# Optimization experiments

Measured on AMD Instinct MI355X. Metric: run time of the kernel, lower is better.

Reference implementation:

```python
import jax, jax.numpy as jnp
import numpy as np


def _to_complex(e):
    # e: [..., L, 2] (real, imag) -> complex64 [..., L]
    return e[..., 0] + 1j * e[..., 1]


def _idct_last(x, expk):
    # IDCT (DCT-III-like, no normalization, full weight on x_0) along last axis:
    #   y_u = sum_{k=0}^{N-1} x_k cos(pi*k*(2u+1)/(2N))
    # Makhoul FFT algorithm: t = N*ifft(x * exp(i*pi*k/(2N)));
    #   y_{2n} = Re t_n, y_{2n+1} = Re t_{N-1-n}
    N = x.shape[-1]
    t = jnp.fft.ifft(x * expk, axis=-1) * N
    re = jnp.real(t).astype(x.dtype)
    y = jnp.zeros_like(x)
    y = y.at[..., 0::2].set(re[..., : (N + 1) // 2])
    y = y.at[..., 1::2].set(re[..., ::-1][..., : N // 2])
    return y


def _idxst_last(x, expk):
    # IDXST along last axis: y_u = sum_{k=0}^{N-1} x_k sin(pi*k*(2u+1)/(2N))
    # Identity: sin(pi*k*(2u+1)/(2N)) = (-1)^u cos(pi*(N-k)*(2u+1)/(2N))
    # => y = (-1)^u * idct(x') with x'_0 = 0, x'_j = x_{N-j}
    N = x.shape[-1]
    xp = jnp.concatenate([jnp.zeros_like(x[..., :1]), x[..., :0:-1]], axis=-1)
    sign = jnp.where(jnp.arange(N) % 2 == 0, 1.0, -1.0).astype(x.dtype)
    return _idct_last(xp, expk) * sign


def setup_inputs() -> dict:
    key = jax.random.key(0)
    M, N = 4096, 4096
    x = jax.random.normal(key, (M, N), dtype=jnp.float32)
    kM = np.arange(M)
    kN = np.arange(N)
    expkM = np.stack([np.cos(np.pi * kM / (2 * M)), np.sin(np.pi * kM / (2 * M))], axis=-1).astype(np.float32)
    expkN = np.stack([np.cos(np.pi * kN / (2 * N)), np.sin(np.pi * kN / (2 * N))], axis=-1).astype(np.float32)
    return {"x": x, "expkM": jnp.asarray(expkM), "expkN": jnp.asarray(expkN)}


def reference(x, expkM, expkN):
    # 2D separable transform: IDXST along dim 0 (M), IDCT along dim 1 (N)
    eM = _to_complex(expkM)
    eN = _to_complex(expkN)
    y = _idxst_last(x.T, eM).T  # idxst over rows (size M)
    y = _idct_last(y, eN)       # idct over cols (size N)
    return y
```

## Files before the change

kernel.cpp:

```cpp
#include <hip/hip_runtime.h>
#include <hip/hip_bf16.h>

typedef __bf16 bf16x8 __attribute__((ext_vector_type(8)));
typedef float  f32x4  __attribute__((ext_vector_type(4)));

__device__ __forceinline__ unsigned short f2bf(float f) {
    union { float f; unsigned int u; } v; v.f = f;
    unsigned int r = v.u + 0x7FFFu + ((v.u >> 16) & 1u);
    return (unsigned short)(r >> 16);
}

__device__ __forceinline__ void async16(const unsigned short* g, unsigned short* l) {
    __builtin_amdgcn_global_load_lds(
        (const __attribute__((address_space(1))) unsigned int*)g,
        (__attribute__((address_space(3))) unsigned int*)l,
        16, 0, 0);
}

__global__ __launch_bounds__(256) void transpose_perm(
    const float* __restrict__ X, unsigned short* __restrict__ Xt, int Mr, int Nc)
{
    __shared__ float tile[64][65];
    const int bx = blockIdx.x * 64;
    const int by = blockIdx.y * 64;
    const int tid = threadIdx.x;
    const int halfM = Mr >> 1;

    const int c4 = (tid & 15) * 4;
    const int r  = tid >> 4;
#pragma unroll
    for (int p = 0; p < 4; ++p) {
        const float4 v = *reinterpret_cast<const float4*>(
            &X[(size_t)(by + r + 16 * p) * Nc + bx + c4]);
        tile[r + 16 * p][c4 + 0] = v.x;
        tile[r + 16 * p][c4 + 1] = v.y;
        tile[r + 16 * p][c4 + 2] = v.z;
        tile[r + 16 * p][c4 + 3] = v.w;
    }
    __syncthreads();

    const int q  = tid & 7;
    const int h  = (tid >> 3) & 1;
    const int n0 = tid >> 4;
#pragma unroll
    for (int p = 0; p < 4; ++p) {
        const int n = n0 + 16 * p;
        ushort4 o;
        o.x = f2bf(tile[8 * q + 0 + h][n]);
        o.y = f2bf(tile[8 * q + 2 + h][n]);
        o.z = f2bf(tile[8 * q + 4 + h][n]);
        o.w = f2bf(tile[8 * q + 6 + h][n]);
        *reinterpret_cast<ushort4*>(
            Xt + (size_t)(bx + n) * Mr + h * halfM + (by >> 1) + 4 * q) = o;
    }
}

__global__ __launch_bounds__(256) void gen_w(
    unsigned short* __restrict__ out, int doSin)
{
    const int flat = (int)(((size_t)blockIdx.x * 256 + threadIdx.x) * 4);
    const int r  = flat >> 12;
    const int c0 = flat & 4095;
    const unsigned int step = 2u * (unsigned int)r + 1u;
    const float scale = 3.14159265358979323846f / 8192.0f;
    unsigned short o[4];
#pragma unroll
    for (int j = 0; j < 4; ++j) {
        const int c = c0 + j;
        const unsigned int kk = (c < 2048) ? (unsigned int)(2 * c)
                                           : (unsigned int)(2 * (c - 2048) + 1);
        unsigned int p = (kk * step) & 16383u;
        float ang = (float)p * scale;
        float v = doSin ? __sinf(ang) : __cosf(ang);
        o[j] = f2bf(v);
    }
    uint2 pack;
    pack.x = (unsigned int)o[0] | ((unsigned int)o[1] << 16);
    pack.y = (unsigned int)o[2] | ((unsigned int)o[3] << 16);
    *reinterpret_cast<uint2*>(out + flat) = pack;
}

#define BARRIER __builtin_amdgcn_s_barrier()
#define LGKM0 asm volatile("s_waitcnt lgkmcnt(0)" ::: "memory")
#define VM6 asm volatile("s_waitcnt vmcnt(6)" ::: "memory")
#define VM0 asm volatile("s_waitcnt vmcnt(0)" ::: "memory")
#define PRIO1 __builtin_amdgcn_s_setprio(1)
#define PRIO0 __builtin_amdgcn_s_setprio(0)

#define STAGE_ALL(LB, KC) do { \
    _Pragma("unroll") for (int U = 0; U < BMU; ++U) \
        async16(pA + (size_t)U * 64 * 4096 + (KC), &lds[(LB) + U * 4096 + ldst]); \
    _Pragma("unroll") for (int U = 0; U < BNU; ++U) \
        async16(pB + (size_t)U * 64 * 4096 + (KC), &lds[(LB) + (BMU + U) * 4096 + ldst]); } while (0)

#define LD_ALL(LB) do { \
    _Pragma("unroll") for (int mm = 0; mm < 4; ++mm) { \
        af[mm][0] = *(const bf16x8*)&lds[(LB) + aOff + mm * 1024 + sl0]; \
        af[mm][1] = *(const bf16x8*)&lds[(LB) + aOff + mm * 1024 + sl1]; } \
    _Pragma("unroll") for (int nn = 0; nn < 4; ++nn) { \
        bfr[nn][0] = *(const bf16x8*)&lds[(LB) + bOff + nn * 1024 + sl0]; \
        bfr[nn][1] = *(const bf16x8*)&lds[(LB) + bOff + nn * 1024 + sl1]; } } while (0)

#define MFMA_ALL(ACC) do { \
    _Pragma("unroll") for (int ks = 0; ks < 2; ++ks) \
    _Pragma("unroll") for (int mm = 0; mm < 4; ++mm) \
    _Pragma("unroll") for (int nn = 0; nn < 4; ++nn) \
        ACC[mm][nn] = __builtin_amdgcn_mfma_f32_16x16x32_bf16( \
            af[mm][ks], bfr[nn][ks], ACC[mm][nn], 0, 0, 0); } while (0)

template <int BMU, int BNU, int EPI, typename OutT>
__global__ __launch_bounds__(512, 2) void gemm_fused(
    const unsigned short* __restrict__ P,
    const unsigned short* __restrict__ Q,
    OutT* __restrict__ C)
{
    __shared__ __align__(16) unsigned short lds[3 * 6 * 4096];

    const int tid  = threadIdx.x;
    const int lane = tid & 63;
    const int w    = tid >> 6;
    const int wm   = w / BNU;
    const int wn   = w % BNU;

    const int bid = blockIdx.x;
    const int wg  = (bid & 7) * 32 + (bid >> 3);
    const int brow = (wg >> 4) * (BMU * 64);
    const int bcol = (wg & 15) * (BNU * 64);

    const int srow = tid >> 3;
    const int sxor = ((tid & 7) ^ (srow & 7)) << 3;
    const unsigned short* pA = P + (size_t)(brow + srow) * 4096 + sxor;
    const unsigned short* pB = Q + (size_t)(bcol + srow) * 4096 + sxor;
    const int ldst = w << 9;

    const int lr = lane & 15, lk = lane >> 4, sx = lr & 7;
    const int sl0 = ((lk) ^ sx) << 3;
    const int sl1 = ((4 + lk) ^ sx) << 3;
    const int aOff = (wm * 64 + lr) * 64;
    const int bOff = BMU * 4096 + (wn * 64 + lr) * 64;

    bf16x8 af[4][2], bfr[4][2];
    f32x4 accE[4][4] = {};
    f32x4 accO[4][4] = {};

    STAGE_ALL(0, 0);
    STAGE_ALL(24576, 64);
    VM6;
    BARRIER;

    int b = 0;
    for (int t = 0; t < 32; ++t) {
        const int lb = b * 24576;
        const int bs = (b >= 1 ? b - 1 : b + 2) * 24576;
        LD_ALL(lb);
        const int tt = t + 2;
        const int kc = ((tt >> 5) << 11) + ((tt & 31) << 6);
        STAGE_ALL(bs, kc);
        PRIO1; MFMA_ALL(accE); PRIO0;
        LGKM0; VM6; BARRIER;
        b = (b == 2) ? 0 : b + 1;
    }
    for (int t = 32; t < 62; ++t) {
        const int lb = b * 24576;
        const int bs = (b >= 1 ? b - 1 : b + 2) * 24576;
        LD_ALL(lb);
        const int tt = t + 2;
        const int kc = ((tt >> 5) << 11) + ((tt & 31) << 6);
        STAGE_ALL(bs, kc);
        PRIO1; MFMA_ALL(accO); PRIO0;
        LGKM0; VM6; BARRIER;
        b = (b == 2) ? 0 : b + 1;
    }
    {
        const int lb = b * 24576;
        LD_ALL(lb);
        PRIO1; MFMA_ALL(accO); PRIO0;
        LGKM0; VM0; BARRIER;
        b = (b == 2) ? 0 : b + 1;
    }
    {
        const int lb = b * 24576;
        LD_ALL(lb);
        PRIO1; MFMA_ALL(accO); PRIO0;
    }

    const int r0 = brow + wm * 64 + (lane >> 4) * 4;
    const int c0 = bcol + wn * 64 + (lane & 15);
#pragma unroll
    for (int mf = 0; mf < 4; ++mf)
#pragma unroll
        for (int nf = 0; nf < 4; ++nf)
#pragma unroll
            for (int r = 0; r < 4; ++r) {
                const int row = r0 + mf * 16 + r;
                const int col = c0 + nf * 16;
                const float e = accE[mf][nf][r];
                const float o = accO[mf][nf][r];
                if (EPI == 1) {
                    const int pin = (col >> 1) + ((col & 1) << 11);
                    ((unsigned short*)C)[(size_t)row * 4096 + pin] = f2bf(e + o);
                    ((unsigned short*)C)[(size_t)(4095 - row) * 4096 + pin] = f2bf(o - e);
                } else {
                    ((float*)C)[(size_t)row * 4096 + col] = e + o;
                    ((float*)C)[(size_t)row * 4096 + 4095 - col] = e - o;
                }
            }
}

extern "C" void kernel_launch(void* const* d_in, const int* in_sizes, int n_in,
                              void* d_out, int out_size, void* d_ws, size_t ws_size,
                              hipStream_t stream) {
    const float* X = (const float*)d_in[0];
    const int Mr = in_sizes[1] / 2;
    const int Nc = in_sizes[2] / 2;

    unsigned short* R0 = (unsigned short*)d_ws;
    unsigned short* R1 = R0 + (size_t)Mr * Nc;
    unsigned short* R2 = R1 + (size_t)(Mr / 2) * Nc;

    transpose_perm<<<dim3(Nc / 64, Mr / 64), 256, 0, stream>>>(X, R0, Mr, Nc);
    gen_w<<<(2048 * 4096 / 4) / 256, 256, 0, stream>>>(R1, 1);
    gemm_fused<2, 4, 1, unsigned short><<<256, 512, 0, stream>>>(R1, R0, R2);
    gen_w<<<(2048 * 4096 / 4) / 256, 256, 0, stream>>>(R1, 0);
    gemm_fused<4, 2, 2, float><<<256, 512, 0, stream>>>(R2, R1, (float*)d_out);
}
```

Measured before the change: 168.3 us.

## Double-buffer MFMA fragments to prefetch next LDS tile during compute

Restructures the GEMM main loop so that each iteration loads register fragments for the next K-tile from LDS while MFMAs run on the current tile's fragments, using two ping-ponged fragment sets. The prologue now stages three tiles before starting, and buffer indices rotate explicitly. The aim is to hide LDS read latency behind matrix math, at the cost of doubled fragment registers, which may pressure occupancy at two blocks per CU or cause spills.

```diff
diff --git a/kernel.cpp b/kernel.cpp
--- a/kernel.cpp
+++ b/kernel.cpp
@@ -93,20 +93,30 @@
     _Pragma("unroll") for (int U = 0; U < BNU; ++U) \
         async16(pB + (size_t)U * 64 * 4096 + (KC), &lds[(LB) + (BMU + U) * 4096 + ldst]); } while (0)
 
-#define LD_ALL(LB) do { \
+#define LDF(AF, BF, LB) do { \
     _Pragma("unroll") for (int mm = 0; mm < 4; ++mm) { \
-        af[mm][0] = *(const bf16x8*)&lds[(LB) + aOff + mm * 1024 + sl0]; \
-        af[mm][1] = *(const bf16x8*)&lds[(LB) + aOff + mm * 1024 + sl1]; } \
+        AF[mm][0] = *(const bf16x8*)&lds[(LB) + aOff + mm * 1024 + sl0]; \
+        AF[mm][1] = *(const bf16x8*)&lds[(LB) + aOff + mm * 1024 + sl1]; } \
     _Pragma("unroll") for (int nn = 0; nn < 4; ++nn) { \
-        bfr[nn][0] = *(const bf16x8*)&lds[(LB) + bOff + nn * 1024 + sl0]; \
-        bfr[nn][1] = *(const bf16x8*)&lds[(LB) + bOff + nn * 1024 + sl1]; } } while (0)
-
-#define MFMA_ALL(ACC) do { \
+        BF[nn][0] = *(const bf16x8*)&lds[(LB) + bOff + nn * 1024 + sl0]; \
+        BF[nn][1] = *(const bf16x8*)&lds[(LB) + bOff + nn * 1024 + sl1]; } } while (0)
+
+#define MFMAF(AF, BF, ACC) do { \
     _Pragma("unroll") for (int ks = 0; ks < 2; ++ks) \
     _Pragma("unroll") for (int mm = 0; mm < 4; ++mm) \
     _Pragma("unroll") for (int nn = 0; nn < 4; ++nn) \
         ACC[mm][nn] = __builtin_amdgcn_mfma_f32_16x16x32_bf16( \
-            af[mm][ks], bfr[nn][ks], ACC[mm][nn], 0, 0, 0); } while (0)
+            AF[mm][ks], BF[nn][ks], ACC[mm][nn], 0, 0, 0); } while (0)
+
+#define ROTATE do { const int _t = lb_cur; lb_cur = lb_nxt; lb_nxt = lb_n2; lb_n2 = _t; } while (0)
+
+#define TILE_PF(FA_N, FB_N, FA_C, FB_C, ACC, TTS, DOSTG, VMW) do { \
+    LDF(FA_N, FB_N, lb_nxt); \
+    if (DOSTG) { const int _kc = (((TTS) >> 5) << 11) + (((TTS) & 31) << 6); \
+                 STAGE_ALL(lb_cur, _kc); } \
+    PRIO1; MFMAF(FA_C, FB_C, ACC); PRIO0; \
+    LGKM0; VMW; BARRIER; \
+    ROTATE; } while (0)
 
 template <int BMU, int BNU, int EPI, typename OutT>
 __global__ __launch_bounds__(512, 2) void gemm_fused(
@@ -139,50 +149,36 @@
     const int aOff = (wm * 64 + lr) * 64;
     const int bOff = BMU * 4096 + (wn * 64 + lr) * 64;
 
-    bf16x8 af[4][2], bfr[4][2];
+    bf16x8 af0[4][2], bf0[4][2];
+    bf16x8 af1[4][2], bf1[4][2];
     f32x4 accE[4][4] = {};
     f32x4 accO[4][4] = {};
 
     STAGE_ALL(0, 0);
     STAGE_ALL(24576, 64);
+    STAGE_ALL(49152, 128);
     VM6;
     BARRIER;
-
-    int b = 0;
-    for (int t = 0; t < 32; ++t) {
-        const int lb = b * 24576;
-        const int bs = (b >= 1 ? b - 1 : b + 2) * 24576;
-        LD_ALL(lb);
-        const int tt = t + 2;
-        const int kc = ((tt >> 5) << 11) + ((tt & 31) << 6);
-        STAGE_ALL(bs, kc);
-        PRIO1; MFMA_ALL(accE); PRIO0;
-        LGKM0; VM6; BARRIER;
-        b = (b == 2) ? 0 : b + 1;
-    }
-    for (int t = 32; t < 62; ++t) {
-        const int lb = b * 24576;
-        const int bs = (b >= 1 ? b - 1 : b + 2) * 24576;
-        LD_ALL(lb);
-        const int tt = t + 2;
-        const int kc = ((tt >> 5) << 11) + ((tt & 31) << 6);
-        STAGE_ALL(bs, kc);
-        PRIO1; MFMA_ALL(accO); PRIO0;
-        LGKM0; VM6; BARRIER;
-        b = (b == 2) ? 0 : b + 1;
-    }
-    {
-        const int lb = b * 24576;
-        LD_ALL(lb);
-        PRIO1; MFMA_ALL(accO); PRIO0;
-        LGKM0; VM0; BARRIER;
-        b = (b == 2) ? 0 : b + 1;
-    }
-    {
-        const int lb = b * 24576;
-        LD_ALL(lb);
-        PRIO1; MFMA_ALL(accO); PRIO0;
-    }
+    LDF(af0, bf0, 0);
+    LGKM0;
+    BARRIER;
+
+    int lb_cur = 0, lb_nxt = 24576, lb_n2 = 49152;
+
+    for (int p = 0; p < 16; ++p) {
+        TILE_PF(af1, bf1, af0, bf0, accE, 2 * p + 3, 1, VM6);
+        TILE_PF(af0, bf0, af1, bf1, accE, 2 * p + 4, 1, VM6);
+    }
+    for (int p = 0; p < 14; ++p) {
+        TILE_PF(af1, bf1, af0, bf0, accO, 2 * p + 35, 1, VM6);
+        TILE_PF(af0, bf0, af1, bf1, accO, 2 * p + 36, 1, VM6);
+    }
+    TILE_PF(af1, bf1, af0, bf0, accO, 63, 1, VM6);
+    TILE_PF(af0, bf0, af1, bf1, accO, 0, 0, VM0);
+    LDF(af1, bf1, lb_nxt);
+    PRIO1; MFMAF(af0, bf0, accO); PRIO0;
+    LGKM0;
+    PRIO1; MFMAF(af1, bf1, accO); PRIO0;
 
     const int r0 = brow + wm * 64 + (lane >> 4) * 4;
     const int c0 = bcol + wn * 64 + (lane & 15);
```

After: 188.9 us. 12.3% more time.

## Shrink GEMM tile to 128x128 with 4-wave blocks and double buffering

Applied to the files above, without the earlier changes.

Both fused GEMMs move from 512-thread blocks computing 128x256 or 256x128 tiles with a triple-buffered, two-deep async prefetch to 256-thread blocks computing 128x128 tiles with a double-buffered, one-deep prefetch. The grid doubles to 512 blocks and the launch bounds allow two blocks per CU, so one CU can overlap two independent blocks instead of relying on a deep pipeline inside one block. Each iteration now waits for all outstanding loads (vmcnt 0), which exposes more global-load latency. The smaller tiles also reduce operand reuse per byte loaded from memory.

```diff
diff --git a/kernel.cpp b/kernel.cpp
--- a/kernel.cpp
+++ b/kernel.cpp
@@ -82,16 +82,13 @@
 
 #define BARRIER __builtin_amdgcn_s_barrier()
 #define LGKM0 asm volatile("s_waitcnt lgkmcnt(0)" ::: "memory")
-#define VM6 asm volatile("s_waitcnt vmcnt(6)" ::: "memory")
 #define VM0 asm volatile("s_waitcnt vmcnt(0)" ::: "memory")
 #define PRIO1 __builtin_amdgcn_s_setprio(1)
 #define PRIO0 __builtin_amdgcn_s_setprio(0)
 
-#define STAGE_ALL(LB, KC) do { \
-    _Pragma("unroll") for (int U = 0; U < BMU; ++U) \
-        async16(pA + (size_t)U * 64 * 4096 + (KC), &lds[(LB) + U * 4096 + ldst]); \
-    _Pragma("unroll") for (int U = 0; U < BNU; ++U) \
-        async16(pB + (size_t)U * 64 * 4096 + (KC), &lds[(LB) + (BMU + U) * 4096 + ldst]); } while (0)
+#define STAGE(LB, KC) do { \
+    _Pragma("unroll") for (int p = 0; p < 8; ++p) \
+        async16(srcp_[p] + (KC), &lds[(LB) + ((p * 256 + wbase) * 8)]); } while (0)
 
 #define LD_ALL(LB) do { \
     _Pragma("unroll") for (int mm = 0; mm < 4; ++mm) { \
@@ -108,78 +105,71 @@
         ACC[mm][nn] = __builtin_amdgcn_mfma_f32_16x16x32_bf16( \
             af[mm][ks], bfr[nn][ks], ACC[mm][nn], 0, 0, 0); } while (0)
 
-template <int BMU, int BNU, int EPI, typename OutT>
-__global__ __launch_bounds__(512, 2) void gemm_fused(
+template <int EPI, typename OutT>
+__global__ __launch_bounds__(256, 2) void gemm_fused(
     const unsigned short* __restrict__ P,
     const unsigned short* __restrict__ Q,
-    OutT* __restrict__ C)
+    OutT* __restrict__ C, int nbx)
 {
-    __shared__ __align__(16) unsigned short lds[3 * 6 * 4096];
+    __shared__ __align__(16) unsigned short lds[2 * 4 * 4096];
 
     const int tid  = threadIdx.x;
     const int lane = tid & 63;
     const int w    = tid >> 6;
-    const int wm   = w / BNU;
-    const int wn   = w % BNU;
+    const int wm   = w >> 1;
+    const int wn   = w & 1;
 
     const int bid = blockIdx.x;
-    const int wg  = (bid & 7) * 32 + (bid >> 3);
-    const int brow = (wg >> 4) * (BMU * 64);
-    const int bcol = (wg & 15) * (BNU * 64);
-
-    const int srow = tid >> 3;
-    const int sxor = ((tid & 7) ^ (srow & 7)) << 3;
-    const unsigned short* pA = P + (size_t)(brow + srow) * 4096 + sxor;
-    const unsigned short* pB = Q + (size_t)(bcol + srow) * 4096 + sxor;
-    const int ldst = w << 9;
+    const int wg  = (bid & 7) * (gridDim.x >> 3) + (bid >> 3);
+    const int brow = (wg / nbx) * 128;
+    const int bcol = (wg % nbx) * 128;
+
+    const unsigned short* srcp_[8];
+    const int wbase = tid & ~63;
+#pragma unroll
+    for (int p = 0; p < 8; ++p) {
+        const int c    = p * 256 + tid;
+        const int unit = c >> 9;
+        const int urow = (c >> 3) & 63;
+        const int slot = c & 7;
+        const int sx   = (slot ^ (urow & 7)) << 3;
+        srcp_[p] = (unit < 2)
+            ? P + (size_t)(brow + unit * 64 + urow) * 4096 + sx
+            : Q + (size_t)(bcol + (unit - 2) * 64 + urow) * 4096 + sx;
+    }
 
     const int lr = lane & 15, lk = lane >> 4, sx = lr & 7;
     const int sl0 = ((lk) ^ sx) << 3;
     const int sl1 = ((4 + lk) ^ sx) << 3;
-    const int aOff = (wm * 64 + lr) * 64;
-    const int bOff = BMU * 4096 + (wn * 64 + lr) * 64;
+    const int aOff = wm * 4096 + lr * 64;
+    const int bOff = (2 + wn) * 4096 + lr * 64;
 
     bf16x8 af[4][2], bfr[4][2];
     f32x4 accE[4][4] = {};
     f32x4 accO[4][4] = {};
 
-    STAGE_ALL(0, 0);
-    STAGE_ALL(24576, 64);
-    VM6;
+    STAGE(0, 0);
+    VM0;
     BARRIER;
 
-    int b = 0;
     for (int t = 0; t < 32; ++t) {
-        const int lb = b * 24576;
-        const int bs = (b >= 1 ? b - 1 : b + 2) * 24576;
+        const int lb = (t & 1) << 14;
+        const int nb = lb ^ 16384;
+        STAGE(nb, (t + 1) << 6);
         LD_ALL(lb);
-        const int tt = t + 2;
-        const int kc = ((tt >> 5) << 11) + ((tt & 31) << 6);
-        STAGE_ALL(bs, kc);
         PRIO1; MFMA_ALL(accE); PRIO0;
-        LGKM0; VM6; BARRIER;
-        b = (b == 2) ? 0 : b + 1;
-    }
-    for (int t = 32; t < 62; ++t) {
-        const int lb = b * 24576;
-        const int bs = (b >= 1 ? b - 1 : b + 2) * 24576;
-        LD_ALL(lb);
-        const int tt = t + 2;
-        const int kc = ((tt >> 5) << 11) + ((tt & 31) << 6);
-        STAGE_ALL(bs, kc);
-        PRIO1; MFMA_ALL(accO); PRIO0;
-        LGKM0; VM6; BARRIER;
-        b = (b == 2) ? 0 : b + 1;
-    }
-    {
-        const int lb = b * 24576;
+        LGKM0; VM0; BARRIER;
+    }
+    for (int t = 32; t < 63; ++t) {
+        const int lb = (t & 1) << 14;
+        const int nb = lb ^ 16384;
+        STAGE(nb, (t + 1) << 6);
         LD_ALL(lb);
         PRIO1; MFMA_ALL(accO); PRIO0;
         LGKM0; VM0; BARRIER;
-        b = (b == 2) ? 0 : b + 1;
     }
     {
-        const int lb = b * 24576;
+        const int lb = (63 & 1) << 14;
         LD_ALL(lb);
         PRIO1; MFMA_ALL(accO); PRIO0;
     }
@@ -220,7 +210,7 @@
 
     transpose_perm<<<dim3(Nc / 64, Mr / 64), 256, 0, stream>>>(X, R0, Mr, Nc);
     gen_w<<<(2048 * 4096 / 4) / 256, 256, 0, stream>>>(R1, 1);
-    gemm_fused<2, 4, 1, unsigned short><<<256, 512, 0, stream>>>(R1, R0, R2);
+    gemm_fused<1, unsigned short><<<512, 256, 0, stream>>>(R1, R0, R2, 32);
     gen_w<<<(2048 * 4096 / 4) / 256, 256, 0, stream>>>(R1, 0);
-    gemm_fused<4, 2, 2, float><<<256, 512, 0, stream>>>(R2, R1, (float*)d_out);
-}
+    gemm_fused<2, float><<<512, 256, 0, stream>>>(R2, R1, (float*)d_out, 16);
+}
```

New measurement: 168.2 us (median of 2 runs). Within noise of the previous version (-0.1%).
